# Performance work log

Measured on AMD Instinct MI355X. Metric: run time of the kernel, lower is better.

## Reference

```python
import jax, jax.numpy as jnp
import numpy as np

B, T, D = 64, 4096, 256
UNITS = 256  # must equal D due to the module's build() wiring


def setup_inputs() -> dict:
    key = jax.random.key(0)
    k1, k2, k3 = jax.random.split(key, 3)
    inputs = jax.random.normal(k1, (B, T, D), dtype=jnp.float32)
    # Glorot-uniform-ish init for Dense kernels, zeros for biases (Keras defaults)
    lim_w = np.sqrt(6.0 / (D + UNITS)).astype(np.float32)
    W_w = jax.random.uniform(k2, (D, UNITS), jnp.float32, -lim_w, lim_w)
    W_b = jnp.zeros((UNITS,), jnp.float32)
    lim_v = np.sqrt(6.0 / (UNITS + 1)).astype(np.float32)
    V_w = jax.random.uniform(k3, (UNITS, 1), jnp.float32, -lim_v, lim_v)
    V_b = jnp.zeros((1,), jnp.float32)
    return {"inputs": inputs, "W_w": W_w, "W_b": W_b, "V_w": V_w, "V_b": V_b}


def reference(inputs, W_w, W_b, V_w, V_b):
    # score: [B, T, UNITS]
    score = jnp.tanh(jnp.einsum('btd,du->btu', inputs, W_w) + W_b)
    # logits: [B, T, 1]; softmax over time axis (axis=1)
    logits = jnp.einsum('btu,uo->bto', score, V_w) + V_b
    attn = jax.nn.softmax(logits, axis=1)  # [B, T, 1]
    # weighted sum over time -> [B, D]
    context = jnp.sum(attn * inputs, axis=1)
    return context
```

## Files before the change

### kernel.cpp

```cpp
#include <hip/hip_runtime.h>
#include <hip/hip_bf16.h>
#include <math.h>

#define BB 64
#define TT 4096
#define DD 256
#define UU 256
#define MT 32
#define NT (TT/MT)
#define TPB 8
#define NBLK (BB*NT/TPB)
#define NP (NT/TPB)
#define LDA 264

typedef __attribute__((ext_vector_type(8))) short bf16x8;
typedef __attribute__((ext_vector_type(4))) float f32x4;

static __device__ __forceinline__ short f2bf(float f){
  unsigned u = __float_as_uint(f);
  u = (u + 0x7fffu + ((u >> 16) & 1u)) >> 16;
  return (short)u;
}

static __device__ __forceinline__ unsigned pk_bf16(float a, float b){
#if __has_builtin(__builtin_amdgcn_cvt_pk_bf16_f32)
  typedef __bf16 bf16v2 __attribute__((ext_vector_type(2)));
  bf16v2 r = __builtin_amdgcn_cvt_pk_bf16_f32(a, b);
  unsigned u; __builtin_memcpy(&u, &r, 4); return u;
#else
  unsigned ua = __float_as_uint(a), ub = __float_as_uint(b);
  ua = (ua + 0x7fffu + ((ua >> 16) & 1u)) >> 16;
  ub = (ub + 0x7fffu + ((ub >> 16) & 1u)) & 0xffff0000u;
  return ub | ua;
#endif
}

__global__ void wfrag_kernel(const float* __restrict__ W, short* __restrict__ Wf){
  int g  = blockIdx.x*256 + threadIdx.x;
  int l  = g & 63;
  int f  = g >> 6;
  int kt = f & 7, nf = (f >> 3) & 3, wv = f >> 5;
  int lo = l & 15, quad = l >> 4;
  int u  = wv*64 + nf*16 + lo;
  int d0 = kt*32 + quad*8;
  bf16x8 v;
  #pragma unroll
  for (int j=0;j<8;++j) v[j] = f2bf(W[(size_t)(d0+j)*UU + u]);
  *reinterpret_cast<bf16x8*>(&Wf[(size_t)g*8]) = v;
}

__global__ __launch_bounds__(256, 2)
void attn_tile_kernel(const float* __restrict__ X, const short* __restrict__ Wf,
                      const float* __restrict__ Wb, const float* __restrict__ Vw,
                      float* __restrict__ m_part, float* __restrict__ l_part,
                      float* __restrict__ ctx_part)
{
  __shared__ short a_tile[2][MT*LDA];
  __shared__ float s_part[4][MT];
  __shared__ float s_pw[4][MT];
  __shared__ float s_red[8][264];

  const int tid  = threadIdx.x;
  const int lane = tid & 63;
  const int wv   = tid >> 6;
  const int lo   = lane & 15;
  const int quad = lane >> 4;
  const int u_base = wv*64 + lo;
  const int blk = blockIdx.x;
  const int b   = blk >> 4;
  const int seg = blk & 15;
  const size_t xbase0 = ((size_t)b*TT + (size_t)(seg*TPB)*MT)*DD;
  const int rgrp  = tid >> 5;
  const int cbase = (tid & 31)*8;

  float wb_r[4], v_r[4];
  #pragma unroll
  for (int nf=0; nf<4; ++nf){
    wb_r[nf] = Wb[u_base + nf*16];
    v_r[nf]  = Vw[u_base + nf*16];
  }

  bf16x8 wreg[4][8];
  {
    const short* wf_base = Wf + ((size_t)(wv*32*64 + lane))*8;
    #pragma unroll
    for (int nf=0; nf<4; ++nf)
      #pragma unroll
      for (int kt=0; kt<8; ++kt)
        wreg[nf][kt] = *reinterpret_cast<const bf16x8*>(wf_base + (nf*8 + kt)*512);
  }

  float4 xp[8];
  #pragma unroll
  for (int p8=0; p8<4; ++p8){
    const float4* src = reinterpret_cast<const float4*>(
        X + xbase0 + (size_t)(p8*8 + rgrp)*DD + cbase);
    xp[p8*2]   = src[0];
    xp[p8*2+1] = src[1];
  }

  float m_run = -INFINITY, l_run = 0.f;
  float cp[8] = {0.f,0.f,0.f,0.f,0.f,0.f,0.f,0.f};

  for (int it=0; it<TPB; ++it){
    const int buf = it & 1;

    #pragma unroll
    for (int p8=0; p8<4; ++p8){
      int4 v;
      v.x = (int)pk_bf16(xp[p8*2].x,   xp[p8*2].y);
      v.y = (int)pk_bf16(xp[p8*2].z,   xp[p8*2].w);
      v.z = (int)pk_bf16(xp[p8*2+1].x, xp[p8*2+1].y);
      v.w = (int)pk_bf16(xp[p8*2+1].z, xp[p8*2+1].w);
      *reinterpret_cast<int4*>(&a_tile[buf][(p8*8 + rgrp)*LDA + cbase]) = v;
    }
    __syncthreads();

    if (it+1 < TPB){
      const size_t xb = xbase0 + (size_t)(it+1)*MT*DD;
      #pragma unroll
      for (int p8=0; p8<4; ++p8){
        const float4* src = reinterpret_cast<const float4*>(
            X + xb + (size_t)(p8*8 + rgrp)*DD + cbase);
        xp[p8*2]   = src[0];
        xp[p8*2+1] = src[1];
      }
    }

    f32x4 acc[2][4];
    #pragma unroll
    for (int mf=0; mf<2; ++mf)
      #pragma unroll
      for (int nf=0; nf<4; ++nf)
        acc[mf][nf] = (f32x4){0.f,0.f,0.f,0.f};

    #pragma unroll
    for (int kt=0; kt<8; ++kt){
      const int k0 = kt*32 + quad*8;
      bf16x8 af[2];
      #pragma unroll
      for (int mf=0; mf<2; ++mf)
        af[mf] = *reinterpret_cast<const bf16x8*>(&a_tile[buf][(mf*16 + lo)*LDA + k0]);
      #pragma unroll
      for (int nf=0; nf<4; ++nf){
        #pragma unroll
        for (int mf=0; mf<2; ++mf)
          acc[mf][nf] = __builtin_amdgcn_mfma_f32_16x16x32_bf16(af[mf], wreg[nf][kt], acc[mf][nf], 0, 0, 0);
      }
    }

    #pragma unroll
    for (int mf=0; mf<2; ++mf){
      #pragma unroll
      for (int r=0; r<4; ++r){
        float part = 0.f;
        #pragma unroll
        for (int nf=0; nf<4; ++nf){
          float s  = acc[mf][nf][r] + wb_r[nf];
          float e2 = __expf(2.f*s);
          float th = 1.f - 2.f/(e2 + 1.f);
          part = fmaf(th, v_r[nf], part);
        }
        part += __shfl_xor(part, 1);
        part += __shfl_xor(part, 2);
        part += __shfl_xor(part, 4);
        part += __shfl_xor(part, 8);
        if (lo == 0) s_part[wv][mf*16 + quad*4 + r] = part;
      }
    }
    __syncthreads();

    const int li = lane & 31;
    float lt = s_part[0][li] + s_part[1][li] + s_part[2][li] + s_part[3][li];
    float mx = lt;
    #pragma unroll
    for (int o=16; o; o>>=1) mx = fmaxf(mx, __shfl_xor(mx, o));

    float m_new = fmaxf(m_run, mx);
    float corr  = __expf(m_run - m_new);
    float p = __expf(lt - m_new);
    float sum = p;
    #pragma unroll
    for (int o=16; o; o>>=1) sum += __shfl_xor(sum, o);
    l_run = l_run * corr + sum;
    s_pw[wv][li] = p;

    if (corr != 1.f){
      #pragma unroll
      for (int j=0; j<8; ++j) cp[j] *= corr;
    }
    m_run = m_new;

    #pragma unroll
    for (int p8=0; p8<4; ++p8){
      float pr = s_pw[wv][p8*8 + rgrp];
      bf16x8 xv = *reinterpret_cast<const bf16x8*>(&a_tile[buf][(p8*8 + rgrp)*LDA + cbase]);
      #pragma unroll
      for (int j=0; j<8; ++j){
        float x = __uint_as_float(((unsigned)(unsigned short)xv[j]) << 16);
        cp[j] = fmaf(pr, x, cp[j]);
      }
    }
  }

  *reinterpret_cast<float4*>(&s_red[rgrp][cbase])   = (float4){cp[0],cp[1],cp[2],cp[3]};
  *reinterpret_cast<float4*>(&s_red[rgrp][cbase+4]) = (float4){cp[4],cp[5],cp[6],cp[7]};
  __syncthreads();

  float ctx = 0.f;
  #pragma unroll
  for (int g=0; g<8; ++g) ctx += s_red[g][tid];

  if (tid == 0){ m_part[blk] = m_run; l_part[blk] = l_run; }
  ctx_part[(size_t)blk*DD + tid] = ctx;
}

__global__ __launch_bounds__(256)
void merge_kernel(const float* __restrict__ m_part, const float* __restrict__ l_part,
                  const float* __restrict__ ctx_part, float* __restrict__ out)
{
  const int b = blockIdx.x;
  const int d = threadIdx.x;

  float mg = -INFINITY;
  #pragma unroll
  for (int i=0; i<NP; ++i) mg = fmaxf(mg, m_part[b*NP+i]);

  float lg = 0.f, s = 0.f;
  #pragma unroll
  for (int i=0; i<NP; ++i){
    float w = __expf(m_part[b*NP+i] - mg);
    lg += l_part[b*NP+i] * w;
    s   = fmaf(w, ctx_part[(size_t)(b*NP+i)*DD + d], s);
  }
  out[b*DD + d] = s / lg;
}

extern "C" void kernel_launch(void* const* d_in, const int* in_sizes, int n_in,
                              void* d_out, int out_size, void* d_ws, size_t ws_size,
                              hipStream_t stream)
{
  const float* X  = (const float*)d_in[0];
  const float* Ww = (const float*)d_in[1];
  const float* Wb = (const float*)d_in[2];
  const float* Vw = (const float*)d_in[3];
  float* out = (float*)d_out;

  short* Wf       = (short*)d_ws;
  float* m_part   = (float*)((char*)d_ws + (size_t)UU*DD*sizeof(short));
  float* l_part   = m_part + NBLK;
  float* ctx_part = l_part + NBLK;

  wfrag_kernel<<<32, 256, 0, stream>>>(Ww, Wf);
  attn_tile_kernel<<<NBLK, 256, 0, stream>>>(X, Wf, Wb, Vw, m_part, l_part, ctx_part);
  merge_kernel<<<BB, 256, 0, stream>>>(m_part, l_part, ctx_part, out);
}
```

Measured before the change: 382.1 us.

## Fuse merge into tile kernel via last-block atomic counter, nontemporal X loads

Removes the separate merge kernel launch. Each tile block now increments a per-batch atomic counter, and the last block to finish for a batch does the log-sum-exp merge and writes the output. The counters are zeroed in the weight-fragment kernel. X loads become nontemporal, the first prefetch is issued before the weight register loads, and the next-tile prefetch moves ahead of the barrier so more memory work overlaps. This saves one launch and gap at the cost of atomics, fences, and a serial merge tail in the last block per batch.

```diff
diff --git a/kernel.cpp b/kernel.cpp
--- a/kernel.cpp
+++ b/kernel.cpp
@@ -35,7 +35,9 @@
 #endif
 }
 
-__global__ void wfrag_kernel(const float* __restrict__ W, short* __restrict__ Wf){
+__global__ void wfrag_kernel(const float* __restrict__ W, short* __restrict__ Wf,
+                             unsigned* __restrict__ cnt){
+  if (blockIdx.x == 0 && threadIdx.x < BB) cnt[threadIdx.x] = 0u;
   int g  = blockIdx.x*256 + threadIdx.x;
   int l  = g & 63;
   int f  = g >> 6;
@@ -53,12 +55,14 @@
 void attn_tile_kernel(const float* __restrict__ X, const short* __restrict__ Wf,
                       const float* __restrict__ Wb, const float* __restrict__ Vw,
                       float* __restrict__ m_part, float* __restrict__ l_part,
-                      float* __restrict__ ctx_part)
+                      float* __restrict__ ctx_part, unsigned* __restrict__ cnt,
+                      float* __restrict__ out)
 {
   __shared__ short a_tile[2][MT*LDA];
   __shared__ float s_part[4][MT];
   __shared__ float s_pw[4][MT];
   __shared__ float s_red[8][264];
+  __shared__ unsigned s_tk;
 
   const int tid  = threadIdx.x;
   const int lane = tid & 63;
@@ -73,6 +77,15 @@
   const int rgrp  = tid >> 5;
   const int cbase = (tid & 31)*8;
 
+  f32x4 xp[8];
+  #pragma unroll
+  for (int p8=0; p8<4; ++p8){
+    const f32x4* src = reinterpret_cast<const f32x4*>(
+        X + xbase0 + (size_t)(p8*8 + rgrp)*DD + cbase);
+    xp[p8*2]   = __builtin_nontemporal_load(src);
+    xp[p8*2+1] = __builtin_nontemporal_load(src+1);
+  }
+
   float wb_r[4], v_r[4];
   #pragma unroll
   for (int nf=0; nf<4; ++nf){
@@ -90,15 +103,6 @@
         wreg[nf][kt] = *reinterpret_cast<const bf16x8*>(wf_base + (nf*8 + kt)*512);
   }
 
-  float4 xp[8];
-  #pragma unroll
-  for (int p8=0; p8<4; ++p8){
-    const float4* src = reinterpret_cast<const float4*>(
-        X + xbase0 + (size_t)(p8*8 + rgrp)*DD + cbase);
-    xp[p8*2]   = src[0];
-    xp[p8*2+1] = src[1];
-  }
-
   float m_run = -INFINITY, l_run = 0.f;
   float cp[8] = {0.f,0.f,0.f,0.f,0.f,0.f,0.f,0.f};
 
@@ -108,24 +112,24 @@
     #pragma unroll
     for (int p8=0; p8<4; ++p8){
       int4 v;
-      v.x = (int)pk_bf16(xp[p8*2].x,   xp[p8*2].y);
-      v.y = (int)pk_bf16(xp[p8*2].z,   xp[p8*2].w);
-      v.z = (int)pk_bf16(xp[p8*2+1].x, xp[p8*2+1].y);
-      v.w = (int)pk_bf16(xp[p8*2+1].z, xp[p8*2+1].w);
+      v.x = (int)pk_bf16(xp[p8*2][0],   xp[p8*2][1]);
+      v.y = (int)pk_bf16(xp[p8*2][2],   xp[p8*2][3]);
+      v.z = (int)pk_bf16(xp[p8*2+1][0], xp[p8*2+1][1]);
+      v.w = (int)pk_bf16(xp[p8*2+1][2], xp[p8*2+1][3]);
       *reinterpret_cast<int4*>(&a_tile[buf][(p8*8 + rgrp)*LDA + cbase]) = v;
     }
-    __syncthreads();
 
     if (it+1 < TPB){
       const size_t xb = xbase0 + (size_t)(it+1)*MT*DD;
       #pragma unroll
       for (int p8=0; p8<4; ++p8){
-        const float4* src = reinterpret_cast<const float4*>(
+        const f32x4* src = reinterpret_cast<const f32x4*>(
             X + xb + (size_t)(p8*8 + rgrp)*DD + cbase);
-        xp[p8*2]   = src[0];
-        xp[p8*2+1] = src[1];
-      }
-    }
+        xp[p8*2]   = __builtin_nontemporal_load(src);
+        xp[p8*2+1] = __builtin_nontemporal_load(src+1);
+      }
+    }
+    __syncthreads();
 
     f32x4 acc[2][4];
     #pragma unroll
@@ -211,29 +215,38 @@
   #pragma unroll
   for (int g=0; g<8; ++g) ctx += s_red[g][tid];
 
+  ctx_part[(size_t)blk*DD + tid] = ctx;
   if (tid == 0){ m_part[blk] = m_run; l_part[blk] = l_run; }
-  ctx_part[(size_t)blk*DD + tid] = ctx;
-}
-
-__global__ __launch_bounds__(256)
-void merge_kernel(const float* __restrict__ m_part, const float* __restrict__ l_part,
-                  const float* __restrict__ ctx_part, float* __restrict__ out)
-{
-  const int b = blockIdx.x;
-  const int d = threadIdx.x;
-
-  float mg = -INFINITY;
-  #pragma unroll
-  for (int i=0; i<NP; ++i) mg = fmaxf(mg, m_part[b*NP+i]);
-
-  float lg = 0.f, s = 0.f;
-  #pragma unroll
-  for (int i=0; i<NP; ++i){
-    float w = __expf(m_part[b*NP+i] - mg);
-    lg += l_part[b*NP+i] * w;
-    s   = fmaf(w, ctx_part[(size_t)(b*NP+i)*DD + d], s);
-  }
-  out[b*DD + d] = s / lg;
+
+  __threadfence();
+  if (tid == 0)
+    s_tk = __hip_atomic_fetch_add(&cnt[b], 1u, __ATOMIC_ACQ_REL,
+                                  __HIP_MEMORY_SCOPE_AGENT);
+  __syncthreads();
+  if (s_tk == NP-1){
+    __threadfence();
+    const int base = b*NP;
+    float mv[NP];
+    float mg = -INFINITY;
+    #pragma unroll
+    for (int i=0; i<NP; ++i){
+      mv[i] = __hip_atomic_load(&m_part[base+i], __ATOMIC_RELAXED,
+                                __HIP_MEMORY_SCOPE_AGENT);
+      mg = fmaxf(mg, mv[i]);
+    }
+    float lg = 0.f, s = 0.f;
+    #pragma unroll
+    for (int i=0; i<NP; ++i){
+      float w  = __expf(mv[i] - mg);
+      float lv = __hip_atomic_load(&l_part[base+i], __ATOMIC_RELAXED,
+                                   __HIP_MEMORY_SCOPE_AGENT);
+      float cv = __hip_atomic_load(&ctx_part[(size_t)(base+i)*DD + tid],
+                                   __ATOMIC_RELAXED, __HIP_MEMORY_SCOPE_AGENT);
+      lg += lv * w;
+      s   = fmaf(w, cv, s);
+    }
+    out[b*DD + tid] = s / lg;
+  }
 }
 
 extern "C" void kernel_launch(void* const* d_in, const int* in_sizes, int n_in,
@@ -250,8 +263,9 @@
   float* m_part   = (float*)((char*)d_ws + (size_t)UU*DD*sizeof(short));
   float* l_part   = m_part + NBLK;
   float* ctx_part = l_part + NBLK;
-
-  wfrag_kernel<<<32, 256, 0, stream>>>(Ww, Wf);
-  attn_tile_kernel<<<NBLK, 256, 0, stream>>>(X, Wf, Wb, Vw, m_part, l_part, ctx_part);
-  merge_kernel<<<BB, 256, 0, stream>>>(m_part, l_part, ctx_part, out);
-}
+  unsigned* cnt   = (unsigned*)(ctx_part + (size_t)NBLK*DD);
+
+  wfrag_kernel<<<32, 256, 0, stream>>>(Ww, Wf, cnt);
+  attn_tile_kernel<<<NBLK, 256, 0, stream>>>(X, Wf, Wb, Vw, m_part, l_part,
+                                             ctx_part, cnt, out);
+}
```

New measurement: 575.0 us. +50.5%, slower.
